# Kernel optimization log

Hardware: AMD Instinct MI355X
Metric: run time of the kernel (lower is better)

The kernel has to match this reference:

```python
import jax, jax.numpy as jnp
import numpy as np

EPS = 1e-8  # torch F.cosine_similarity eps


def _mp_cos(p, q, w):
    # multi-perspective cosine: p,q (b,s,h), w (l,h) -> (b,s,l)
    pw = p[:, None, :, :] * w[None, :, None, :]   # (b,l,s,h)
    qw = q[:, None, :, :] * w[None, :, None, :]
    num = jnp.sum(pw * qw, axis=-1)
    den = jnp.maximum(jnp.linalg.norm(pw, axis=-1) * jnp.linalg.norm(qw, axis=-1), EPS)
    return (num / den).transpose(0, 2, 1)          # (b,s,l)


def _full(p, q, w, direction):
    # match every step of p against last (fw) / first (bw) step of q
    q_t = q[:, -1, :] if direction == 'fw' else q[:, 0, :]
    return _mp_cos(p, jnp.broadcast_to(q_t[:, None, :], p.shape), w)


def _maxpool(p, q, w):
    pw = p[:, None, :, :] * w[None, :, None, :]    # (b,l,sp,h)
    qw = q[:, None, :, :] * w[None, :, None, :]    # (b,l,sq,h)
    dot = jnp.einsum('blph,blqh->blpq', pw, qw)
    mag = jnp.linalg.norm(pw, axis=-1)[..., None] * jnp.linalg.norm(qw, axis=-1)[:, :, None, :]
    cos = (dot / mag).transpose(0, 2, 3, 1)        # (b,sp,sq,l)
    return cos.max(axis=2), cos.max(axis=1)        # (b,sp,l), (b,sq,l)


def _attentive(p, q, w, att):
    pn = jnp.linalg.norm(p, axis=2)                # (b,sp)
    qn = jnp.linalg.norm(q, axis=2)                # (b,sq)
    cos = jnp.einsum('bph,bqh->bpq', p, q) / (pn[:, :, None] * qn[:, None, :])
    if att == 'mean':
        # weighted sums without materializing (b,sp,sq,h)
        p_vec = jnp.einsum('bph,bpq->bqh', p, cos) / cos.sum(axis=1)[..., None]  # (b,sq,h)
        q_vec = jnp.einsum('bqh,bpq->bph', q, cos) / cos.sum(axis=2)[..., None]  # (b,sp,h)
    else:  # 'max' -- elementwise max requires the broadcasted tensor
        p_vec = (p[:, :, None, :] * cos[..., None]).max(axis=1)  # (b,sq,h)
        q_vec = (q[:, None, :, :] * cos[..., None]).max(axis=2)  # (b,sp,h)
    return _mp_cos(p, q_vec, w), _mp_cos(q, p_vec, w)


def _forward(p, q, W):
    h = W.shape[-1]
    pf, pb = p[..., :h], p[..., h:]
    qf, qb = q[..., :h], q[..., h:]
    mv_p, mv_q = [], []
    # full matching
    mv_p += [_full(pf, qf, W[0], 'fw'), _full(pb, qb, W[1], 'bw')]
    mv_q += [_full(qf, pf, W[0], 'fw'), _full(qb, pb, W[1], 'bw')]
    # maxpool matching
    pp_f, pq_f = _maxpool(pf, qf, W[2])
    pp_b, pq_b = _maxpool(pb, qb, W[3])
    mv_p += [pp_f, pp_b]
    mv_q += [pq_f, pq_b]
    # attentive (mean) matching
    ap_f, aq_f = _attentive(pf, qf, W[4], 'mean')
    ap_b, aq_b = _attentive(pb, qb, W[5], 'mean')
    mv_p += [ap_f, ap_b]
    mv_q += [aq_f, aq_b]
    # max-attentive matching
    mp_f, mq_f = _attentive(pf, qf, W[6], 'max')
    mp_b, mq_b = _attentive(pb, qb, W[7], 'max')
    mv_p += [mp_f, mp_b]
    mv_q += [mq_f, mq_b]
    # dropout is identity at inference (training=False)
    return jnp.concatenate(mv_p, axis=2), jnp.concatenate(mv_q, axis=2)


def setup_inputs() -> dict:
    key = jax.random.key(0)
    k1, k2, k3 = jax.random.split(key, 3)
    B, S, H, L = 32, 64, 300, 20
    p = jax.random.normal(k1, (B, S, 2 * H), dtype=jnp.float32)
    q = jax.random.normal(k2, (B, S, 2 * H), dtype=jnp.float32)
    W = jax.random.uniform(k3, (8, L, H), dtype=jnp.float32)  # torch.rand init
    return {"p": p, "q": q, "W": W}


def reference(p, q, W):
    return _forward(p, q, W)
```

## Files before the change

kernel.cpp:

```cpp
#include <hip/hip_runtime.h>

#define B_ 32
#define S_ 64
#define H_ 300
#define H2_ 600
#define L_ 20
#define ROW_ 160
#define OUTQ_OFF ((size_t)B_ * S_ * ROW_)
#define NEG_INF -3.402823466e38f

#define NB_MP 1280
#define NB_W 188
#define NB_COS 1024

typedef __attribute__((ext_vector_type(8))) _Float16 half8v;
typedef __attribute__((ext_vector_type(4))) _Float16 half4v;
typedef __attribute__((ext_vector_type(4))) float float4v;
typedef __attribute__((ext_vector_type(2))) float float2v;

struct CosS {
  float xq[S_][65];
  float xp[4][68];
  float qn_l[S_];
  float cp[4][S_];
};

__device__ __forceinline__ void cos_body(char* smem, int bid,
                                         const float* __restrict__ P,
                                         const float* __restrict__ Q,
                                         float* __restrict__ cosM,
                                         float* __restrict__ sumpart,
                                         float* __restrict__ sum_q) {
  CosS& S = *(CosS*)smem;
  int x = bid & 7, j = bid >> 3;
  int bd = x + 8 * (j & 7);
  int pg = bid >> 6;
  int b = bd >> 1, dir = bd & 1;
  int t = threadIdx.x;
  int q = t & 63, pr = t >> 6;
  const float* Pb = P + (size_t)b * S_ * H2_ + dir * H_;
  const float* Qb = Q + (size_t)b * S_ * H2_ + dir * H_;
  float dot = 0.f, np2 = 0.f, nq2 = 0.f;
  for (int c0 = 0; c0 < H_; c0 += 64) {
    __syncthreads();
#pragma unroll
    for (int jj = 0; jj < 4; ++jj) {
      int idx = t + 256 * jj;
      int s = idx >> 4, g = idx & 15;
      int h = c0 + 4 * g;
      float4v v = {0.f, 0.f, 0.f, 0.f};
      if (h < 297) v = *(const float4v*)&Qb[(size_t)s * H2_ + h];
      S.xq[s][4 * g + 0] = v.x; S.xq[s][4 * g + 1] = v.y;
      S.xq[s][4 * g + 2] = v.z; S.xq[s][4 * g + 3] = v.w;
    }
    if (t < 64) {
      int s = t >> 4, g = t & 15;
      int h = c0 + 4 * g;
      float4v v = {0.f, 0.f, 0.f, 0.f};
      if (h < 297) v = *(const float4v*)&Pb[(size_t)(pg * 4 + s) * H2_ + h];
      *(float4v*)&S.xp[s][4 * g] = v;
    }
    __syncthreads();
    for (int hh = 0; hh < 64; hh += 4) {
      float4v av = *(const float4v*)&S.xp[pr][hh];
      float q0 = S.xq[q][hh + 0];
      float q1 = S.xq[q][hh + 1];
      float q2 = S.xq[q][hh + 2];
      float q3 = S.xq[q][hh + 3];
      dot = fmaf(av.x, q0, dot); dot = fmaf(av.y, q1, dot);
      dot = fmaf(av.z, q2, dot); dot = fmaf(av.w, q3, dot);
      np2 = fmaf(av.x, av.x, np2); np2 = fmaf(av.y, av.y, np2);
      np2 = fmaf(av.z, av.z, np2); np2 = fmaf(av.w, av.w, np2);
      if (pr == 0) {
        nq2 = fmaf(q0, q0, nq2); nq2 = fmaf(q1, q1, nq2);
        nq2 = fmaf(q2, q2, nq2); nq2 = fmaf(q3, q3, nq2);
      }
    }
  }
  if (pr == 0) S.qn_l[q] = sqrtf(nq2);
  __syncthreads();
  float pn = sqrtf(np2);
  float c = dot / (pn * S.qn_l[q]);
  int p = pg * 4 + pr;
  cosM[(size_t)bd * S_ * S_ + (size_t)p * S_ + q] = c;
  float rs = c;
#pragma unroll
  for (int m = 1; m < 64; m <<= 1) rs += __shfl_xor(rs, m);
  if (q == 0) sum_q[bd * S_ + p] = rs;
  S.cp[pr][q] = c;
  __syncthreads();
  if (t < S_)
    sumpart[((size_t)bd * 16 + pg) * S_ + t] =
        S.cp[0][t] + S.cp[1][t] + S.cp[2][t] + S.cp[3][t];
}

#define HP 72
struct MaxpoolS {
  _Float16 ph[S_][HP];
  _Float16 qh[S_][HP];
  float w1s[H_];
  float pn2[S_], qn2[S_];
  float colp[4][S_];
};

__device__ __forceinline__ void maxpool_body(char* smem, int bid,
                                             const float* __restrict__ P,
                                             const float* __restrict__ Q,
                                             const float* __restrict__ Wf,
                                             float* __restrict__ out) {
  MaxpoolS& S = *(MaxpoolS*)smem;
  int x = bid & 7, j = bid >> 3;
  int bd = x + 8 * (j & 7);
  int l = j >> 3;
  int b = bd >> 1, dir = bd & 1;
  int t = threadIdx.x;
  int w = t >> 6, lane = t & 63, quad = lane >> 4, col = lane & 15;
  const float* wg = Wf + (size_t)(2 + dir) * L_ * H_ + (size_t)l * H_;
  if (t < 75) {
    float4v v = *(const float4v*)&wg[4 * t];
    float4v a = {fabsf(v.x), fabsf(v.y), fabsf(v.z), fabsf(v.w)};
    *(float4v*)&S.w1s[4 * t] = a;
  }
  const float* Pb = P + (size_t)b * S_ * H2_ + dir * H_;
  const float* Qb = Q + (size_t)b * S_ * H2_ + dir * H_;
  float4v acc[4];
#pragma unroll
  for (int qt = 0; qt < 4; ++qt) acc[qt] = (float4v){0.f, 0.f, 0.f, 0.f};
  float np2a[4] = {0.f, 0.f, 0.f, 0.f};
  float nq2a[4] = {0.f, 0.f, 0.f, 0.f};
  for (int h0 = 0; h0 < H_; h0 += 64) {
    __syncthreads();
#pragma unroll
    for (int jj = 0; jj < 4; ++jj) {
      int idx = t + 256 * jj;
      int s = idx >> 4, c4 = idx & 15;
      int h = h0 + 4 * c4;
      float4v pv = {0.f, 0.f, 0.f, 0.f}, qv = {0.f, 0.f, 0.f, 0.f};
      if (h < 297) {
        float4v wv = *(const float4v*)&S.w1s[h];
        float4v p4 = *(const float4v*)&Pb[(size_t)s * H2_ + h];
        float4v q4 = *(const float4v*)&Qb[(size_t)s * H2_ + h];
        pv = p4 * wv;
        qv = q4 * wv;
      }
      half4v phv = __builtin_convertvector(pv, half4v);
      half4v qhv = __builtin_convertvector(qv, half4v);
      *(half4v*)&S.ph[s][4 * c4] = phv;
      *(half4v*)&S.qh[s][4 * c4] = qhv;
      float4v pf = __builtin_convertvector(phv, float4v);
      float4v qf = __builtin_convertvector(qhv, float4v);
      np2a[jj] += pf.x * pf.x + pf.y * pf.y + pf.z * pf.z + pf.w * pf.w;
      nq2a[jj] += qf.x * qf.x + qf.y * qf.y + qf.z * qf.z + qf.w * qf.w;
    }
    __syncthreads();
#pragma unroll
    for (int ks = 0; ks < 2; ++ks) {
      half8v ah = *(const half8v*)&S.ph[16 * w + col][ks * 32 + quad * 8];
#pragma unroll
      for (int qt = 0; qt < 4; ++qt) {
        half8v bh = *(const half8v*)&S.qh[16 * qt + col][ks * 32 + quad * 8];
        acc[qt] = __builtin_amdgcn_mfma_f32_16x16x32_f16(ah, bh, acc[qt], 0, 0, 0);
      }
    }
  }
#pragma unroll
  for (int jj = 0; jj < 4; ++jj) {
    float a = np2a[jj], bb = nq2a[jj];
#pragma unroll
    for (int m = 1; m < 16; m <<= 1) {
      a += __shfl_xor(a, m);
      bb += __shfl_xor(bb, m);
    }
    if ((t & 15) == 0) {
      int s = (t >> 4) + 16 * jj;
      S.pn2[s] = a;
      S.qn2[s] = bb;
    }
  }
  __syncthreads();
  float pnv[4];
#pragma unroll
  for (int r = 0; r < 4; ++r) pnv[r] = sqrtf(S.pn2[16 * w + quad * 4 + r]);
  float rowm[4] = {NEG_INF, NEG_INF, NEG_INF, NEG_INF};
#pragma unroll
  for (int qt = 0; qt < 4; ++qt) {
    float qnv = sqrtf(S.qn2[16 * qt + col]);
    float cmv = NEG_INF;
#pragma unroll
    for (int r = 0; r < 4; ++r) {
      float c = acc[qt][r] / (pnv[r] * qnv);
      rowm[r] = fmaxf(rowm[r], c);
      cmv = fmaxf(cmv, c);
    }
    cmv = fmaxf(cmv, __shfl_xor(cmv, 16));
    cmv = fmaxf(cmv, __shfl_xor(cmv, 32));
    if (quad == 0) S.colp[w][16 * qt + col] = cmv;
  }
#pragma unroll
  for (int m = 1; m < 16; m <<= 1)
#pragma unroll
    for (int r = 0; r < 4; ++r) rowm[r] = fmaxf(rowm[r], __shfl_xor(rowm[r], m));
  if (col == 0) {
#pragma unroll
    for (int r = 0; r < 4; ++r) {
      int p = 16 * w + quad * 4 + r;
      out[((size_t)b * S_ + p) * ROW_ + (2 + dir) * L_ + l] = rowm[r];
    }
  }
  __syncthreads();
  if (t < S_) {
    float m0 = fmaxf(fmaxf(S.colp[0][t], S.colp[1][t]), fmaxf(S.colp[2][t], S.colp[3][t]));
    out[OUTQ_OFF + ((size_t)b * S_ + t) * ROW_ + (2 + dir) * L_ + l] = m0;
  }
}

__global__ __launch_bounds__(256) void k1(const float* __restrict__ P,
                                          const float* __restrict__ Q,
                                          const float* __restrict__ Wf,
                                          float* __restrict__ w2r,
                                          float* __restrict__ cosM,
                                          float* __restrict__ sumpart,
                                          float* __restrict__ sum_q,
                                          float* __restrict__ out) {
  extern __shared__ char smem[];
  int bid = blockIdx.x;
  if (bid < NB_MP) {
    maxpool_body(smem, bid, P, Q, Wf, out);
  } else if (bid < NB_MP + NB_W) {
    int i = (bid - NB_MP) * 256 + threadIdx.x;
    if (i < 8 * L_ * H_) {
      float v = Wf[i];
      w2r[i] = v * v;
    }
  } else {
    cos_body(smem, bid - (NB_MP + NB_W), P, Q, cosM, sumpart, sum_q);
  }
}

#define SG 4
struct OutsS {
  float u[600];
  float ttq[300], ttp[300];
  float xP[SG][H_], xQ[SG][H_];
  float vmq[SG][H_], vmp[SG][H_], vxq[SG][H_], vxp[SG][H_];
  float sps[SG], sqs[SG];
};

__device__ __forceinline__ void outs_tail_job(const OutsS& S, int l, int pr,
                                              int si, int dir, int b, int s0,
                                              const float* __restrict__ w2r,
                                              float* __restrict__ out) {
  const float* xv = (pr & 1) ? S.xQ[si] : S.xP[si];
  const float* y;
  if (pr == 0) y = S.ttq;
  else if (pr == 1) y = S.ttp;
  else if (pr == 2) y = S.vmq[si];
  else if (pr == 3) y = S.vmp[si];
  else if (pr == 4) y = S.vxq[si];
  else y = S.vxp[si];
  const int wb_[6] = {0, 0, 4, 4, 6, 6};
  int widx = wb_[pr] + dir;
  const float* wp = w2r + (size_t)widx * (L_ * H_) + (size_t)l * H_;
  float4v a1v = {0.f, 0.f, 0.f, 0.f};
  float4v a2v = {0.f, 0.f, 0.f, 0.f};
  float4v a3v = {0.f, 0.f, 0.f, 0.f};
  for (int h4 = 0; h4 < H_; h4 += 4) {
    float4v wv = *(const float4v*)&wp[h4];
    float4v xx = *(const float4v*)&xv[h4];
    float4v yy = *(const float4v*)&y[h4];
    float4v wx = wv * xx;
    float4v wy = wv * yy;
    a1v = wx * yy + a1v;
    a2v = wx * xx + a2v;
    a3v = wy * yy + a3v;
  }
  float a1 = (a1v.x + a1v.y) + (a1v.z + a1v.w);
  float a2 = (a2v.x + a2v.y) + (a2v.z + a2v.w);
  float a3 = (a3v.x + a3v.y) + (a3v.z + a3v.w);
  float den = fmaxf(sqrtf(a2) * sqrtf(a3), 1e-8f);
  float c = a1 / den;
  int s = s0 + si;
  size_t base = ((pr & 1) ? OUTQ_OFF : 0) + ((size_t)b * S_ + s) * ROW_;
  out[base + (size_t)widx * L_ + l] = c;
}

__global__ __launch_bounds__(512) void k2(const float* __restrict__ P,
                                          const float* __restrict__ Q,
                                          const float* __restrict__ w2r,
                                          const float* __restrict__ cosM,
                                          const float* __restrict__ sumpart,
                                          const float* __restrict__ sum_q,
                                          float* __restrict__ out) {
  extern __shared__ char smem[];
  OutsS& S = *(OutsS*)smem;
  int bid = blockIdx.x;
  int x = bid & 7, j = bid >> 3;
  int bd = x + 8 * (j & 7);
  int sg = j >> 3;
  int s0 = sg * SG;
  int b = bd >> 1, dir = bd & 1;
  int t = threadIdx.x;
  int tgt = dir ? 0 : S_ - 1;
  const float* Pb = P + (size_t)b * S_ * H2_ + dir * H_;
  const float* Qb = Q + (size_t)b * S_ * H2_ + dir * H_;
  float (*cosT)[8] = (float (*)[8])&S.u[0];
  const float* cm = cosM + (size_t)bd * S_ * S_;
  {
    int k = t >> 3, jj = t & 7, si = jj & 3;
    cosT[k][jj] = (jj < 4) ? cm[(size_t)k * S_ + s0 + si]
                           : cm[(size_t)(s0 + si) * S_ + k];
  }
  if (t < SG * 75) {
    int si = t / 75, c4 = t - si * 75;
    *(float4v*)&S.xP[si][4 * c4] = *(const float4v*)&Pb[(size_t)(s0 + si) * H2_ + 4 * c4];
    *(float4v*)&S.xQ[si][4 * c4] = *(const float4v*)&Qb[(size_t)(s0 + si) * H2_ + 4 * c4];
  } else if (t < 375) {
    int i = t - 300;
    *(float4v*)&S.ttq[4 * i] = *(const float4v*)&Qb[(size_t)tgt * H2_ + 4 * i];
  } else if (t < 450) {
    int i = t - 375;
    *(float4v*)&S.ttp[4 * i] = *(const float4v*)&Pb[(size_t)tgt * H2_ + 4 * i];
  } else if (t < 454) {
    float a = 0.f;
    int si = t - 450;
    for (int pg = 0; pg < 16; ++pg) a += sumpart[((size_t)bd * 16 + pg) * S_ + s0 + si];
    S.sps[si] = a;
  } else if (t < 458) {
    S.sqs[t - 454] = sum_q[bd * S_ + s0 + (t - 454)];
  }
  __syncthreads();
  if (t < H_) {
    int h = t;
    float2v amp01 = {0.f, 0.f}, amp23 = {0.f, 0.f};
    float2v amq01 = {0.f, 0.f}, amq23 = {0.f, 0.f};
    float2v axp01 = {NEG_INF, NEG_INF}, axp23 = {NEG_INF, NEG_INF};
    float2v axq01 = {NEG_INF, NEG_INF}, axq23 = {NEG_INF, NEG_INF};
#pragma unroll 4
    for (int k = 0; k < S_; ++k) {
      float pv = Pb[(size_t)k * H2_ + h];
      float qv = Qb[(size_t)k * H2_ + h];
      float4v cc = *(const float4v*)&cosT[k][0];
      float4v cr = *(const float4v*)&cosT[k][4];
      float2v cc01 = {cc.x, cc.y}, cc23 = {cc.z, cc.w};
      float2v cr01 = {cr.x, cr.y}, cr23 = {cr.z, cr.w};
      float2v m0 = pv * cc01;
      amp01 += m0; axp01 = __builtin_elementwise_max(axp01, m0);
      float2v m1 = pv * cc23;
      amp23 += m1; axp23 = __builtin_elementwise_max(axp23, m1);
      float2v m2 = qv * cr01;
      amq01 += m2; axq01 = __builtin_elementwise_max(axq01, m2);
      float2v m3 = qv * cr23;
      amq23 += m3; axq23 = __builtin_elementwise_max(axq23, m3);
    }
    S.vmq[0][h] = amq01.x / S.sqs[0];
    S.vmq[1][h] = amq01.y / S.sqs[1];
    S.vmq[2][h] = amq23.x / S.sqs[2];
    S.vmq[3][h] = amq23.y / S.sqs[3];
    S.vmp[0][h] = amp01.x / S.sps[0];
    S.vmp[1][h] = amp01.y / S.sps[1];
    S.vmp[2][h] = amp23.x / S.sps[2];
    S.vmp[3][h] = amp23.y / S.sps[3];
    S.vxq[0][h] = axq01.x; S.vxq[1][h] = axq01.y;
    S.vxq[2][h] = axq23.x; S.vxq[3][h] = axq23.y;
    S.vxp[0][h] = axp01.x; S.vxp[1][h] = axp01.y;
    S.vxp[2][h] = axp23.x; S.vxp[3][h] = axp23.y;
  } else if (t >= 320 && t < 480) {
    int jb = t - 320;
    int l = jb >> 3, g = jb & 7;
    int pr = g >> 2, si = g & 3;
    outs_tail_job(S, l, pr, si, dir, b, s0, w2r, out);
  }
  __syncthreads();
  if (t < 320) {
    int l = t >> 4, g = t & 15;
    int pr = 2 + (g >> 2), si = g & 3;
    outs_tail_job(S, l, pr, si, dir, b, s0, w2r, out);
  }
}

extern "C" void kernel_launch(void* const* d_in, const int* in_sizes, int n_in,
                              void* d_out, int out_size, void* d_ws, size_t ws_size,
                              hipStream_t stream) {
  (void)out_size; (void)ws_size;
  int iw = 2;
  for (int i = 0; i < n_in; ++i) if (in_sizes[i] == 8 * L_ * H_) iw = i;
  int io[2] = {0, 1}, k = 0;
  for (int i = 0; i < n_in && k < 2; ++i) if (i != iw) io[k++] = i;
  const float* P  = (const float*)d_in[io[0]];
  const float* Q  = (const float*)d_in[io[1]];
  const float* Wf = (const float*)d_in[iw];
  float* out = (float*)d_out;

  float* ws = (float*)d_ws;
  float* w2r     = ws;
  float* cosM    = w2r + 48000;
  float* sumpart = cosM + 262144;
  float* sum_q   = sumpart + 65536;

  size_t sh1 = sizeof(CosS) > sizeof(MaxpoolS) ? sizeof(CosS) : sizeof(MaxpoolS);
  k1<<<NB_MP + NB_W + NB_COS, 256, sh1, stream>>>(P, Q, Wf, w2r, cosM, sumpart, sum_q, out);
  k2<<<B_ * 2 * 16, 512, sizeof(OutsS), stream>>>(P, Q, w2r, cosM, sumpart, sum_q, out);
}
```

Before: 137.1 us.

## Compute attention cosine matrix with fp16 MFMA, one block per batch-direction

Replaces the 1024-block scalar-FMA cosine kernel with 64 blocks that each compute the full 64x64 cosine matrix for one (batch, direction) using 16x16x32 f16 MFMA. Row and column sums are reduced inside the block, so k2 reads a single sum_p value instead of adding 16 partial sums. This cuts redundant reloading of Q across p-groups and the number of blocks. In exchange, the dot products use fp16 inputs, which lowers accuracy; the norms are taken from the fp16-rounded values to stay consistent.

```diff
diff --git a/kernel.cpp b/kernel.cpp
--- a/kernel.cpp
+++ b/kernel.cpp
@@ -11,90 +11,15 @@
 
 #define NB_MP 1280
 #define NB_W 188
-#define NB_COS 1024
+#define NB_CM 64
 
 typedef __attribute__((ext_vector_type(8))) _Float16 half8v;
 typedef __attribute__((ext_vector_type(4))) _Float16 half4v;
 typedef __attribute__((ext_vector_type(4))) float float4v;
 typedef __attribute__((ext_vector_type(2))) float float2v;
 
-struct CosS {
-  float xq[S_][65];
-  float xp[4][68];
-  float qn_l[S_];
-  float cp[4][S_];
-};
-
-__device__ __forceinline__ void cos_body(char* smem, int bid,
-                                         const float* __restrict__ P,
-                                         const float* __restrict__ Q,
-                                         float* __restrict__ cosM,
-                                         float* __restrict__ sumpart,
-                                         float* __restrict__ sum_q) {
-  CosS& S = *(CosS*)smem;
-  int x = bid & 7, j = bid >> 3;
-  int bd = x + 8 * (j & 7);
-  int pg = bid >> 6;
-  int b = bd >> 1, dir = bd & 1;
-  int t = threadIdx.x;
-  int q = t & 63, pr = t >> 6;
-  const float* Pb = P + (size_t)b * S_ * H2_ + dir * H_;
-  const float* Qb = Q + (size_t)b * S_ * H2_ + dir * H_;
-  float dot = 0.f, np2 = 0.f, nq2 = 0.f;
-  for (int c0 = 0; c0 < H_; c0 += 64) {
-    __syncthreads();
-#pragma unroll
-    for (int jj = 0; jj < 4; ++jj) {
-      int idx = t + 256 * jj;
-      int s = idx >> 4, g = idx & 15;
-      int h = c0 + 4 * g;
-      float4v v = {0.f, 0.f, 0.f, 0.f};
-      if (h < 297) v = *(const float4v*)&Qb[(size_t)s * H2_ + h];
-      S.xq[s][4 * g + 0] = v.x; S.xq[s][4 * g + 1] = v.y;
-      S.xq[s][4 * g + 2] = v.z; S.xq[s][4 * g + 3] = v.w;
-    }
-    if (t < 64) {
-      int s = t >> 4, g = t & 15;
-      int h = c0 + 4 * g;
-      float4v v = {0.f, 0.f, 0.f, 0.f};
-      if (h < 297) v = *(const float4v*)&Pb[(size_t)(pg * 4 + s) * H2_ + h];
-      *(float4v*)&S.xp[s][4 * g] = v;
-    }
-    __syncthreads();
-    for (int hh = 0; hh < 64; hh += 4) {
-      float4v av = *(const float4v*)&S.xp[pr][hh];
-      float q0 = S.xq[q][hh + 0];
-      float q1 = S.xq[q][hh + 1];
-      float q2 = S.xq[q][hh + 2];
-      float q3 = S.xq[q][hh + 3];
-      dot = fmaf(av.x, q0, dot); dot = fmaf(av.y, q1, dot);
-      dot = fmaf(av.z, q2, dot); dot = fmaf(av.w, q3, dot);
-      np2 = fmaf(av.x, av.x, np2); np2 = fmaf(av.y, av.y, np2);
-      np2 = fmaf(av.z, av.z, np2); np2 = fmaf(av.w, av.w, np2);
-      if (pr == 0) {
-        nq2 = fmaf(q0, q0, nq2); nq2 = fmaf(q1, q1, nq2);
-        nq2 = fmaf(q2, q2, nq2); nq2 = fmaf(q3, q3, nq2);
-      }
-    }
-  }
-  if (pr == 0) S.qn_l[q] = sqrtf(nq2);
-  __syncthreads();
-  float pn = sqrtf(np2);
-  float c = dot / (pn * S.qn_l[q]);
-  int p = pg * 4 + pr;
-  cosM[(size_t)bd * S_ * S_ + (size_t)p * S_ + q] = c;
-  float rs = c;
-#pragma unroll
-  for (int m = 1; m < 64; m <<= 1) rs += __shfl_xor(rs, m);
-  if (q == 0) sum_q[bd * S_ + p] = rs;
-  S.cp[pr][q] = c;
-  __syncthreads();
-  if (t < S_)
-    sumpart[((size_t)bd * 16 + pg) * S_ + t] =
-        S.cp[0][t] + S.cp[1][t] + S.cp[2][t] + S.cp[3][t];
-}
-
 #define HP 72
+
 struct MaxpoolS {
   _Float16 ph[S_][HP];
   _Float16 qh[S_][HP];
@@ -214,12 +139,123 @@
   }
 }
 
+struct CosmS {
+  _Float16 ph[S_][HP];
+  _Float16 qh[S_][HP];
+  float pn2[S_], qn2[S_];
+  float colp[4][S_];
+};
+
+__device__ __forceinline__ void cosm_body(char* smem, int bd,
+                                          const float* __restrict__ P,
+                                          const float* __restrict__ Q,
+                                          float* __restrict__ cosM,
+                                          float* __restrict__ sum_p,
+                                          float* __restrict__ sum_q) {
+  CosmS& S = *(CosmS*)smem;
+  int b = bd >> 1, dir = bd & 1;
+  int t = threadIdx.x;
+  int w = t >> 6, lane = t & 63, quad = lane >> 4, col = lane & 15;
+  const float* Pb = P + (size_t)b * S_ * H2_ + dir * H_;
+  const float* Qb = Q + (size_t)b * S_ * H2_ + dir * H_;
+  float4v acc[4];
+#pragma unroll
+  for (int qt = 0; qt < 4; ++qt) acc[qt] = (float4v){0.f, 0.f, 0.f, 0.f};
+  float np2a[4] = {0.f, 0.f, 0.f, 0.f};
+  float nq2a[4] = {0.f, 0.f, 0.f, 0.f};
+  for (int h0 = 0; h0 < H_; h0 += 64) {
+    __syncthreads();
+#pragma unroll
+    for (int jj = 0; jj < 4; ++jj) {
+      int idx = t + 256 * jj;
+      int s = idx >> 4, c4 = idx & 15;
+      int h = h0 + 4 * c4;
+      float4v pv = {0.f, 0.f, 0.f, 0.f}, qv = {0.f, 0.f, 0.f, 0.f};
+      if (h < 297) {
+        pv = *(const float4v*)&Pb[(size_t)s * H2_ + h];
+        qv = *(const float4v*)&Qb[(size_t)s * H2_ + h];
+      }
+      half4v phv = __builtin_convertvector(pv, half4v);
+      half4v qhv = __builtin_convertvector(qv, half4v);
+      *(half4v*)&S.ph[s][4 * c4] = phv;
+      *(half4v*)&S.qh[s][4 * c4] = qhv;
+      float4v pf = __builtin_convertvector(phv, float4v);
+      float4v qf = __builtin_convertvector(qhv, float4v);
+      np2a[jj] += pf.x * pf.x + pf.y * pf.y + pf.z * pf.z + pf.w * pf.w;
+      nq2a[jj] += qf.x * qf.x + qf.y * qf.y + qf.z * qf.z + qf.w * qf.w;
+    }
+    __syncthreads();
+#pragma unroll
+    for (int ks = 0; ks < 2; ++ks) {
+      half8v ah = *(const half8v*)&S.ph[16 * w + col][ks * 32 + quad * 8];
+#pragma unroll
+      for (int qt = 0; qt < 4; ++qt) {
+        half8v bh = *(const half8v*)&S.qh[16 * qt + col][ks * 32 + quad * 8];
+        acc[qt] = __builtin_amdgcn_mfma_f32_16x16x32_f16(ah, bh, acc[qt], 0, 0, 0);
+      }
+    }
+  }
+#pragma unroll
+  for (int jj = 0; jj < 4; ++jj) {
+    float a = np2a[jj], bb = nq2a[jj];
+#pragma unroll
+    for (int m = 1; m < 16; m <<= 1) {
+      a += __shfl_xor(a, m);
+      bb += __shfl_xor(bb, m);
+    }
+    if ((t & 15) == 0) {
+      int s = (t >> 4) + 16 * jj;
+      S.pn2[s] = a;
+      S.qn2[s] = bb;
+    }
+  }
+  __syncthreads();
+  float pnv[4];
+#pragma unroll
+  for (int r = 0; r < 4; ++r) pnv[r] = sqrtf(S.pn2[16 * w + quad * 4 + r]);
+  float* cm = cosM + (size_t)bd * S_ * S_;
+  float rows_[4] = {0.f, 0.f, 0.f, 0.f};
+  float cols_[4] = {0.f, 0.f, 0.f, 0.f};
+#pragma unroll
+  for (int qt = 0; qt < 4; ++qt) {
+    float qnv = sqrtf(S.qn2[16 * qt + col]);
+#pragma unroll
+    for (int r = 0; r < 4; ++r) {
+      float c = acc[qt][r] / (pnv[r] * qnv);
+      cm[(size_t)(16 * w + quad * 4 + r) * S_ + 16 * qt + col] = c;
+      rows_[r] += c;
+      cols_[qt] += c;
+    }
+  }
+#pragma unroll
+  for (int m = 1; m < 16; m <<= 1)
+#pragma unroll
+    for (int r = 0; r < 4; ++r) rows_[r] += __shfl_xor(rows_[r], m);
+  if (col == 0) {
+#pragma unroll
+    for (int r = 0; r < 4; ++r)
+      sum_q[bd * S_ + 16 * w + quad * 4 + r] = rows_[r];
+  }
+#pragma unroll
+  for (int qt = 0; qt < 4; ++qt) {
+    cols_[qt] += __shfl_xor(cols_[qt], 16);
+    cols_[qt] += __shfl_xor(cols_[qt], 32);
+  }
+  if (quad == 0) {
+#pragma unroll
+    for (int qt = 0; qt < 4; ++qt) S.colp[w][16 * qt + col] = cols_[qt];
+  }
+  __syncthreads();
+  if (t < S_)
+    sum_p[bd * S_ + t] = S.colp[0][t] + S.colp[1][t] + S.colp[2][t] + S.colp[3][t];
+}
+
 __global__ __launch_bounds__(256) void k1(const float* __restrict__ P,
                                           const float* __restrict__ Q,
                                           const float* __restrict__ Wf,
                                           float* __restrict__ w2r,
                                           float* __restrict__ cosM,
-                                          float* __restrict__ sumpart,
+                                          float* __restrict__ sum_p,
                                           float* __restrict__ sum_q,
                                           float* __restrict__ out) {
   extern __shared__ char smem[];
@@ -233,7 +269,7 @@
       w2r[i] = v * v;
     }
   } else {
-    cos_body(smem, bid - (NB_MP + NB_W), P, Q, cosM, sumpart, sum_q);
+    cosm_body(smem, bid - (NB_MP + NB_W), P, Q, cosM, sum_p, sum_q);
   }
 }
 
@@ -288,7 +324,7 @@
                                           const float* __restrict__ Q,
                                           const float* __restrict__ w2r,
                                           const float* __restrict__ cosM,
-                                          const float* __restrict__ sumpart,
+                                          const float* __restrict__ sum_p,
                                           const float* __restrict__ sum_q,
                                           float* __restrict__ out) {
   extern __shared__ char smem[];
@@ -321,10 +357,7 @@
     int i = t - 375;
     *(float4v*)&S.ttp[4 * i] = *(const float4v*)&Pb[(size_t)tgt * H2_ + 4 * i];
   } else if (t < 454) {
-    float a = 0.f;
-    int si = t - 450;
-    for (int pg = 0; pg < 16; ++pg) a += sumpart[((size_t)bd * 16 + pg) * S_ + s0 + si];
-    S.sps[si] = a;
+    S.sps[t - 450] = sum_p[bd * S_ + s0 + (t - 450)];
   } else if (t < 458) {
     S.sqs[t - 454] = sum_q[bd * S_ + s0 + (t - 454)];
   }
@@ -394,10 +427,10 @@
   float* ws = (float*)d_ws;
   float* w2r     = ws;
   float* cosM    = w2r + 48000;
-  float* sumpart = cosM + 262144;
-  float* sum_q   = sumpart + 65536;
-
-  size_t sh1 = sizeof(CosS) > sizeof(MaxpoolS) ? sizeof(CosS) : sizeof(MaxpoolS);
-  k1<<<NB_MP + NB_W + NB_COS, 256, sh1, stream>>>(P, Q, Wf, w2r, cosM, sumpart, sum_q, out);
-  k2<<<B_ * 2 * 16, 512, sizeof(OutsS), stream>>>(P, Q, w2r, cosM, sumpart, sum_q, out);
-}
+  float* sum_p   = cosM + 262144;
+  float* sum_q   = sum_p + 4096;
+
+  size_t sh1 = sizeof(MaxpoolS);
+  k1<<<NB_MP + NB_W + NB_CM, 256, sh1, stream>>>(P, Q, Wf, w2r, cosM, sum_p, sum_q, out);
+  k2<<<B_ * 2 * 16, 512, sizeof(OutsS), stream>>>(P, Q, w2r, cosM, sum_p, sum_q, out);
+}
```

Result: faster. 129.8 us (-5.4%).
